# Performance work log

Measured on AMD Instinct MI355X. Metric: run time of the kernel, lower is better.

Reference implementation:

```python
import jax, jax.numpy as jnp
import numpy as np

N_PROD, N_CUST = 100000, 50000
HID, OUT = 128, 64
E_PP, E_PC, E_LB = 800000, 800000, 400000


def sage(x_src, x_dst, src, dst, Wl, bl, Wr, n_dst):
    # PyG SAGEConv (mean aggr): lin_l(mean_{j->i} x_j) + lin_r(x_i); bias on lin_l only
    msg = x_src[src]                                             # [E, d] gather
    s = jax.ops.segment_sum(msg, dst, num_segments=n_dst)        # [n_dst, d]
    cnt = jax.ops.segment_sum(jnp.ones((src.shape[0],), x_src.dtype), dst, num_segments=n_dst)
    mean = s / jnp.maximum(cnt, 1.0)[:, None]
    return mean @ Wl.T + bl + x_dst @ Wr.T


def setup_inputs() -> dict:
    key = jax.random.key(0)
    ks = iter(jax.random.split(key, 40))

    def lin_w(i, o):
        return (jax.random.normal(next(ks), (o, i), jnp.float32) / np.sqrt(i))

    inp = {}
    inp['x_product'] = jax.random.normal(next(ks), (N_PROD, HID), jnp.float32)
    inp['x_customer'] = jax.random.normal(next(ks), (N_CUST, HID), jnp.float32)
    inp['ei_pp'] = jax.random.randint(next(ks), (2, E_PP), 0, N_PROD)
    src_pc = jax.random.randint(next(ks), (1, E_PC), 0, N_PROD)
    dst_pc = jax.random.randint(next(ks), (1, E_PC), 0, N_CUST)
    inp['ei_pc'] = jnp.concatenate([src_pc, dst_pc], axis=0)
    row = jax.random.randint(next(ks), (1, E_LB), 0, N_CUST)
    col = jax.random.randint(next(ks), (1, E_LB), 0, N_PROD)
    inp['edge_label_index'] = jnp.concatenate([row, col], axis=0)

    # ItemGNNEncoder params
    inp['it_W1l'], inp['it_W1r'] = lin_w(HID, HID), lin_w(HID, HID)
    inp['it_b1'] = jnp.zeros((HID,), jnp.float32)
    inp['it_W2l'], inp['it_W2r'] = lin_w(HID, HID), lin_w(HID, HID)
    inp['it_b2'] = jnp.zeros((HID,), jnp.float32)
    inp['it_Wlin'] = lin_w(HID, OUT)
    inp['it_blin'] = jnp.zeros((OUT,), jnp.float32)
    # UserGNNEncoder params
    inp['us_W1l'], inp['us_W1r'] = lin_w(HID, HID), lin_w(HID, HID)
    inp['us_b1'] = jnp.zeros((HID,), jnp.float32)
    inp['us_W2l'], inp['us_W2r'] = lin_w(HID, HID), lin_w(HID, HID)
    inp['us_b2'] = jnp.zeros((HID,), jnp.float32)
    inp['us_W3l'], inp['us_W3r'] = lin_w(HID, HID), lin_w(HID, HID)
    inp['us_b3'] = jnp.zeros((HID,), jnp.float32)
    inp['us_Wlin'] = lin_w(HID, OUT)
    inp['us_blin'] = jnp.zeros((OUT,), jnp.float32)
    # EdgeDecoder params
    inp['de_W1'] = lin_w(2 * OUT, OUT)
    inp['de_b1'] = jnp.zeros((OUT,), jnp.float32)
    inp['de_W2'] = lin_w(OUT, 1)
    inp['de_b2'] = jnp.zeros((1,), jnp.float32)
    return inp


def reference(x_product, x_customer, ei_pp, ei_pc, edge_label_index,
              it_W1l, it_b1, it_W1r, it_W2l, it_b2, it_W2r, it_Wlin, it_blin,
              us_W1l, us_b1, us_W1r, us_W2l, us_b2, us_W2r, us_W3l, us_b3, us_W3r,
              us_Wlin, us_blin, de_W1, de_b1, de_W2, de_b2):
    pp_s, pp_d = ei_pp[0], ei_pp[1]
    pc_s, pc_d = ei_pc[0], ei_pc[1]

    # ItemGNNEncoder on product-product metapath
    p = jax.nn.relu(sage(x_product, x_product, pp_s, pp_d, it_W1l, it_b1, it_W1r, N_PROD))
    p = jax.nn.relu(sage(p, p, pp_s, pp_d, it_W2l, it_b2, it_W2r, N_PROD))
    z_prod = p @ it_Wlin.T + it_blin                              # [N_PROD, OUT]

    # UserGNNEncoder
    px = jax.nn.relu(sage(x_product, x_product, pp_s, pp_d, us_W1l, us_b1, us_W1r, N_PROD))
    cx = jax.nn.relu(sage(x_product, x_customer, pc_s, pc_d, us_W2l, us_b2, us_W2r, N_CUST))
    cx = jax.nn.relu(sage(px, cx, pc_s, pc_d, us_W3l, us_b3, us_W3r, N_CUST))
    z_cust = cx @ us_Wlin.T + us_blin                             # [N_CUST, OUT]

    # EdgeDecoder: gather-concat-MLP
    row, col = edge_label_index[0], edge_label_index[1]
    z = jnp.concatenate([z_cust[row], z_prod[col]], axis=-1)      # [E_LB, 2*OUT]
    z = jax.nn.relu(z @ de_W1.T + de_b1)
    return z @ de_W2.T + de_b2                                    # [E_LB, 1]
```

## Files before the change

kernel.cpp:

```cpp
#include <hip/hip_runtime.h>
#include <hip/hip_bf16.h>

#define HID   128
#define OUTD  64
#define NPROD 100000
#define NCUST 50000
#define EPP   800000
#define EPC   800000
#define ELB   400000
#define NBK   391
#define EBLK  4096
#define RCAP3 512
#define BCAP3 2560
#define CPADN 400
#define NB3   392
#define NCAST 6250

typedef __bf16 bf16x8 __attribute__((ext_vector_type(8)));
typedef float  f32x4  __attribute__((ext_vector_type(4)));
typedef unsigned short u16;
typedef unsigned int u32;

__device__ __forceinline__ float b2f(u16 u) {
  unsigned int v = ((unsigned int)u) << 16;
  float f; __builtin_memcpy(&f, &v, 4); return f;
}
__device__ __forceinline__ u16 f2b(float f) {
  __hip_bfloat16 h = __float2bfloat16(f);
  u16 u; __builtin_memcpy(&u, &h, 2); return u;
}

union Pack8 { u16 u[8]; int4 v; };

__device__ __forceinline__ int sidx(int row, int chunk) {
  return row * HID + ((chunk ^ (row & 15)) << 3);
}
__device__ __forceinline__ int sidx64(int row, int chunk) {
  return row * 64 + ((chunk ^ (row & 7)) << 3);
}

#define NJOBS 13
struct CastJobs { const float* src[NJOBS]; int n8[NJOBS]; };

__global__ __launch_bounds__(256) void k_prep(const int* __restrict__ ei_pp,
                                              const int* __restrict__ ei_pc,
                                              int* __restrict__ bfill_pp,
                                              int* __restrict__ bfill_pc,
                                              u32* __restrict__ bss_pp,
                                              u32* __restrict__ bss_pc,
                                              const float* __restrict__ x_prod,
                                              u16* __restrict__ XPB,
                                              CastJobs jobs,
                                              u16* __restrict__ wbuf) {
  __shared__ int lcnt[NBK], lstart[NBK], lfill[NBK], gbase[NBK];
  __shared__ u32 spay[EBLK];
  __shared__ u16 sbk[EBLK];
  __shared__ int wtot[4];
  const int t = threadIdx.x;
  int bid = blockIdx.x;

  if (bid >= NB3) {
    bid -= NB3;
    if (bid < NCAST) {
      int i = bid * 256 + t;
      float4 a = ((const float4*)x_prod)[2 * i];
      float4 b = ((const float4*)x_prod)[2 * i + 1];
      Pack8 p;
      p.u[0] = f2b(a.x); p.u[1] = f2b(a.y); p.u[2] = f2b(a.z); p.u[3] = f2b(a.w);
      p.u[4] = f2b(b.x); p.u[5] = f2b(b.y); p.u[6] = f2b(b.z); p.u[7] = f2b(b.w);
      ((int4*)XPB)[i] = p.v;
      return;
    }
    bid -= NCAST;
    int job = bid >> 3;
    int idx = (bid & 7) * 256 + t;
    int off8 = (job < 10) ? job * 2048 : 10 * 2048 + (job - 10) * 1024;
    if (idx >= jobs.n8[job]) return;
    const float* s = jobs.src[job];
    float4 a = ((const float4*)s)[2 * idx];
    float4 b = ((const float4*)s)[2 * idx + 1];
    Pack8 p;
    p.u[0] = f2b(a.x); p.u[1] = f2b(a.y); p.u[2] = f2b(a.z); p.u[3] = f2b(a.w);
    p.u[4] = f2b(b.x); p.u[5] = f2b(b.y); p.u[6] = f2b(b.z); p.u[7] = f2b(b.w);
    ((int4*)wbuf)[off8 + idx] = p.v;
    return;
  }

  const int lane = t & 63, wv = t >> 6;
  int xcc; asm("s_getreg_b32 %0, hwreg(HW_REG_XCC_ID)" : "=s"(xcc));
  const int rep = xcc & 7;
  const int NBLK_PP = (EPP + EBLK - 1) / EBLK;
  const bool isPP = bid < NBLK_PP;
  const int* ei = isPP ? ei_pp : ei_pc;
  const int E  = isPP ? EPP : EPC;
  const int SH = isPP ? 8 : 7;
  int* bfill = isPP ? bfill_pp : bfill_pc;
  u32* bss   = isPP ? bss_pp : bss_pc;
  const int base = (isPP ? bid : bid - NBLK_PP) * EBLK;
  const int n = min(EBLK, E - base);

  for (int j = t; j < NBK; j += 256) { lcnt[j] = 0; lfill[j] = 0; }
  __syncthreads();

  u32 pay[16]; int bk[16];
  #pragma unroll
  for (int i = 0; i < 16; ++i) {
    int idx = i * 256 + t;
    bk[i] = -1;
    if (idx < n) {
      int e = base + idx;
      int s = ei[e];
      int d = ei[E + e];
      int b = d >> SH;
      bk[i] = b;
      pay[i] = ((u32)s << SH) | (u32)(d & ((1 << SH) - 1));
      atomicAdd(&lcnt[b], 1);
    }
  }
  __syncthreads();
  {
    int a0 = (2 * t < NBK) ? lcnt[2 * t] : 0;
    int a1 = (2 * t + 1 < NBK) ? lcnt[2 * t + 1] : 0;
    int s = a0 + a1;
    #pragma unroll
    for (int d = 1; d < 64; d <<= 1) {
      int u = __shfl_up(s, d, 64);
      if (lane >= d) s += u;
    }
    if (lane == 63) wtot[wv] = s;
    __syncthreads();
    int wpre = 0;
    for (int w = 0; w < wv; ++w) wpre += wtot[w];
    int excl = s + wpre - (a0 + a1);
    if (2 * t < NBK) lstart[2 * t] = excl;
    if (2 * t + 1 < NBK) lstart[2 * t + 1] = excl + a0;
  }
  __syncthreads();
  for (int b = t; b < NBK; b += 256) {
    int c = lcnt[b];
    gbase[b] = c ? atomicAdd(&bfill[(rep * CPADN + b) << 4], c) : 0;
  }
  #pragma unroll
  for (int i = 0; i < 16; ++i) {
    if (bk[i] >= 0) {
      int pos = lstart[bk[i]] + atomicAdd(&lfill[bk[i]], 1);
      spay[pos] = pay[i];
      sbk[pos] = (u16)bk[i];
    }
  }
  __syncthreads();
  for (int i = t; i < n; i += 256) {
    int b = sbk[i];
    int slot = gbase[b] + (i - lstart[b]);
    if (slot < RCAP3)
      bss[(b * 8 + rep) * RCAP3 + slot] = spay[i];
  }
}

__global__ __launch_bounds__(256) void k_bsort2(const u32* __restrict__ bss_pp,
                                                const int* __restrict__ bfill_pp,
                                                const u32* __restrict__ bss_pc,
                                                const int* __restrict__ bfill_pc,
                                                int* __restrict__ gctr,
                                                int* __restrict__ esrc_pp,
                                                int* __restrict__ start_pp,
                                                int* __restrict__ cnt_pp,
                                                int* __restrict__ esrc_pc,
                                                int* __restrict__ start_pc,
                                                int* __restrict__ cnt_pc) {
  __shared__ u32 pairs[BCAP3];
  __shared__ int outsrc[BCAP3];
  __shared__ int lcnt[256], lstart[256], lfill[256];
  __shared__ int sh_n, sh_base, rn[8], roff[8], wtot[4];
  const int tid = threadIdx.x;
  const int lane = tid & 63, wv = tid >> 6;
  const bool isPP = (int)blockIdx.x < NBK;
  const int b = isPP ? (int)blockIdx.x : (int)blockIdx.x - NBK;
  const int K   = isPP ? 256 : 128;
  const int SHL = isPP ? 8 : 7;
  const u32* bss   = isPP ? bss_pp : bss_pc;
  const int* bfill = isPP ? bfill_pp : bfill_pc;
  int* gc    = isPP ? gctr : gctr + 1;
  int* esrc  = isPP ? esrc_pp : esrc_pc;
  int* start = isPP ? start_pp : start_pc;
  int* cnt   = isPP ? cnt_pp : cnt_pc;
  const int n_nodes = isPP ? NPROD : NCUST;

  if (tid < 8) rn[tid] = min(bfill[(tid * CPADN + b) << 4], RCAP3);
  for (int j = tid; j < K; j += 256) { lcnt[j] = 0; lfill[j] = 0; }
  __syncthreads();
  if (tid == 0) {
    int run = 0;
    for (int r = 0; r < 8; ++r) {
      roff[r] = run;
      int m = min(rn[r], BCAP3 - run);
      rn[r] = m;
      run += m;
    }
    sh_n = run;
    sh_base = atomicAdd(gc, run);
  }
  __syncthreads();
  const int n = sh_n, base = sh_base;
  const int Km1 = K - 1;
  #pragma unroll
  for (int r = 0; r < 8; ++r) {
    int m = rn[r], o = roff[r];
    for (int i = tid; i < m; i += 256) {
      u32 p = bss[(b * 8 + r) * RCAP3 + i];
      pairs[o + i] = p;
      atomicAdd(&lcnt[p & Km1], 1);
    }
  }
  __syncthreads();
  {
    int a0 = (2 * tid < K) ? lcnt[2 * tid] : 0;
    int a1 = (2 * tid + 1 < K) ? lcnt[2 * tid + 1] : 0;
    int s = a0 + a1;
    #pragma unroll
    for (int d = 1; d < 64; d <<= 1) {
      int u = __shfl_up(s, d, 64);
      if (lane >= d) s += u;
    }
    if (lane == 63) wtot[wv] = s;
    __syncthreads();
    int wpre = 0;
    for (int w = 0; w < wv; ++w) wpre += wtot[w];
    int excl = s + wpre - (a0 + a1);
    if (2 * tid < K) lstart[2 * tid] = excl;
    if (2 * tid + 1 < K) lstart[2 * tid + 1] = excl + a0;
  }
  __syncthreads();
  for (int i = tid; i < n; i += 256) {
    u32 p = pairs[i];
    int ln = p & Km1;
    int pos = lstart[ln] + atomicAdd(&lfill[ln], 1);
    outsrc[pos] = (int)(p >> SHL);
  }
  __syncthreads();
  for (int i = tid; i < n; i += 256) esrc[base + i] = outsrc[i];
  const int nb0 = b * K;
  for (int j = tid; j < K; j += 256) {
    int g = nb0 + j;
    if (g < n_nodes) { start[g] = base + lstart[j]; cnt[g] = lcnt[j]; }
  }
}

__global__ __launch_bounds__(256) void k_agg2(const int* __restrict__ es_a,
                                              const int* __restrict__ st_a,
                                              const int* __restrict__ cn_a,
                                              const u16* __restrict__ xa,
                                              u16* __restrict__ oa, int na,
                                              const int* __restrict__ es_b,
                                              const int* __restrict__ st_b,
                                              const int* __restrict__ cn_b,
                                              const u16* __restrict__ xb,
                                              u16* __restrict__ ob, int nb, int blkA) {
  const int t = threadIdx.x;
  const bool A = (int)blockIdx.x < blkA;
  const int node = (A ? (int)blockIdx.x : (int)blockIdx.x - blkA) * 16 + (t >> 4);
  const int l16 = t & 15;
  const int q4  = t & 48;
  if (node >= (A ? na : nb)) return;
  const int* esrc  = A ? es_a : es_b;
  const u16* x     = A ? xa : xb;
  u16* outm        = A ? oa : ob;
  int s0 = (A ? st_a : st_b)[node];
  int c  = (A ? cn_a : cn_b)[node];
  float acc[8] = {0.f, 0.f, 0.f, 0.f, 0.f, 0.f, 0.f, 0.f};
  for (int j0 = 0; j0 < c; j0 += 16) {
    int nch = min(16, c - j0);
    int eid = (l16 < nch) ? esrc[s0 + j0 + l16] : 0;
    int k = 0;
    for (; k + 4 <= nch; k += 4) {
      int s0i = __shfl(eid, q4 + k, 64);
      int s1i = __shfl(eid, q4 + k + 1, 64);
      int s2i = __shfl(eid, q4 + k + 2, 64);
      int s3i = __shfl(eid, q4 + k + 3, 64);
      Pack8 p0, p1, p2, p3;
      p0.v = *(const int4*)(x + (size_t)s0i * HID + l16 * 8);
      p1.v = *(const int4*)(x + (size_t)s1i * HID + l16 * 8);
      p2.v = *(const int4*)(x + (size_t)s2i * HID + l16 * 8);
      p3.v = *(const int4*)(x + (size_t)s3i * HID + l16 * 8);
      #pragma unroll
      for (int u = 0; u < 8; ++u)
        acc[u] += (b2f(p0.u[u]) + b2f(p1.u[u])) + (b2f(p2.u[u]) + b2f(p3.u[u]));
    }
    for (; k < nch; ++k) {
      int s = __shfl(eid, q4 + k, 64);
      Pack8 p;
      p.v = *(const int4*)(x + (size_t)s * HID + l16 * 8);
      #pragma unroll
      for (int u = 0; u < 8; ++u) acc[u] += b2f(p.u[u]);
    }
  }
  float inv = 1.0f / (float)max(c, 1);
  Pack8 o;
  #pragma unroll
  for (int u = 0; u < 8; ++u) o.u[u] = f2b(acc[u] * inv);
  *(int4*)(outm + (size_t)node * HID + l16 * 8) = o.v;
}

__global__ __launch_bounds__(256) void k_lay1(
    const u16* __restrict__ cxA1, const u16* __restrict__ cxW1,
    const float* __restrict__ cxA2f, const u16* __restrict__ cxW2,
    const float* __restrict__ cxBias, u16* __restrict__ cxOut, int Mcx,
    const u16* __restrict__ A1, const u16* __restrict__ A2,
    const u16* __restrict__ Wa, const u16* __restrict__ Wb,
    const u16* __restrict__ Wc, const u16* __restrict__ Wd,
    const float* __restrict__ bias1, const float* __restrict__ bias2,
    u16* __restrict__ out1, u16* __restrict__ out2, int M2o,
    int blkCx) {
  __shared__ __align__(16) u16 sA1[64 * HID];
  __shared__ __align__(16) u16 sA2[64 * HID];
  __shared__ __align__(16) u16 sW[128 * HID];
  const int tid  = threadIdx.x;
  const int lane = tid & 63;
  const int wave = tid >> 6;
  const int q    = lane >> 4;
  const int r16  = lane & 15;
  const bool isCx = (int)blockIdx.x < blkCx;

  if (isCx) {
    const int m0 = blockIdx.x * 64;
    f32x4 acc[4][2];
    #pragma unroll
    for (int i = 0; i < 4; ++i)
      #pragma unroll
      for (int j = 0; j < 2; ++j) {
        acc[i][j][0] = 0.f; acc[i][j][1] = 0.f; acc[i][j][2] = 0.f; acc[i][j][3] = 0.f;
      }
    #pragma unroll
    for (int phase = 0; phase < 2; ++phase) {
      const u16* W = phase ? cxW2 : cxW1;
      if (phase) __syncthreads();
      #pragma unroll
      for (int i = 0; i < 4; ++i) {
        int idx = i * 256 + tid;
        int rr = idx >> 4, c8 = idx & 15;
        int gr = m0 + rr;
        Pack8 p; p.v = make_int4(0, 0, 0, 0);
        if (gr < Mcx) {
          if (phase == 0) {
            p.v = *(const int4*)(cxA1 + (size_t)gr * HID + c8 * 8);
          } else {
            const float* s = cxA2f + (size_t)gr * HID + c8 * 8;
            float4 f0 = ((const float4*)s)[0], f1 = ((const float4*)s)[1];
            p.u[0] = f2b(f0.x); p.u[1] = f2b(f0.y); p.u[2] = f2b(f0.z); p.u[3] = f2b(f0.w);
            p.u[4] = f2b(f1.x); p.u[5] = f2b(f1.y); p.u[6] = f2b(f1.z); p.u[7] = f2b(f1.w);
          }
        }
        *(int4*)(sA1 + sidx(rr, c8)) = p.v;
      }
      #pragma unroll
      for (int i = 0; i < 8; ++i) {
        int idx = i * 256 + tid;
        int rr = idx >> 4, c8 = idx & 15;
        *(int4*)(sW + sidx(rr, c8)) = *(const int4*)(W + (size_t)rr * HID + c8 * 8);
      }
      __syncthreads();
      #pragma unroll
      for (int ks = 0; ks < 4; ++ks) {
        int chunk = ks * 4 + q;
        bf16x8 a[4], b[2];
        #pragma unroll
        for (int mi = 0; mi < 4; ++mi)
          a[mi] = *(const bf16x8*)(sA1 + sidx(mi * 16 + r16, chunk));
        #pragma unroll
        for (int ni = 0; ni < 2; ++ni)
          b[ni] = *(const bf16x8*)(sW + sidx(wave * 32 + ni * 16 + r16, chunk));
        #pragma unroll
        for (int mi = 0; mi < 4; ++mi)
          #pragma unroll
          for (int ni = 0; ni < 2; ++ni)
            acc[mi][ni] = __builtin_amdgcn_mfma_f32_16x16x32_bf16(a[mi], b[ni], acc[mi][ni], 0, 0, 0);
      }
    }
    #pragma unroll
    for (int ni = 0; ni < 2; ++ni) {
      int col = wave * 32 + ni * 16 + r16;
      float bv = cxBias[col];
      #pragma unroll
      for (int mi = 0; mi < 4; ++mi)
        #pragma unroll
        for (int r = 0; r < 4; ++r) {
          int gr = m0 + mi * 16 + q * 4 + r;
          if (gr < Mcx)
            cxOut[(size_t)gr * HID + col] = f2b(fmaxf(acc[mi][ni][r] + bv, 0.f));
        }
    }
    return;
  }

  const int m0 = ((int)blockIdx.x - blkCx) * 64;
  f32x4 acc1[4][2], acc2[4][2];
  #pragma unroll
  for (int i = 0; i < 4; ++i)
    #pragma unroll
    for (int j = 0; j < 2; ++j) {
      acc1[i][j][0] = 0.f; acc1[i][j][1] = 0.f; acc1[i][j][2] = 0.f; acc1[i][j][3] = 0.f;
      acc2[i][j][0] = 0.f; acc2[i][j][1] = 0.f; acc2[i][j][2] = 0.f; acc2[i][j][3] = 0.f;
    }

  #pragma unroll
  for (int i = 0; i < 4; ++i) {
    int idx = i * 256 + tid;
    int rr = idx >> 4, c8 = idx & 15;
    int gr = m0 + rr;
    Pack8 p1, p2;
    p1.v = make_int4(0, 0, 0, 0);
    p2.v = make_int4(0, 0, 0, 0);
    if (gr < M2o) {
      p1.v = *(const int4*)(A1 + (size_t)gr * HID + c8 * 8);
      p2.v = *(const int4*)(A2 + (size_t)gr * HID + c8 * 8);
    }
    *(int4*)(sA1 + sidx(rr, c8)) = p1.v;
    *(int4*)(sA2 + sidx(rr, c8)) = p2.v;
  }

  bf16x8 af[4][4];

  auto stageW = [&](const u16* W) {
    #pragma unroll
    for (int i = 0; i < 8; ++i) {
      int idx = i * 256 + tid;
      int rr = idx >> 4, c8 = idx & 15;
      *(int4*)(sW + sidx(rr, c8)) = *(const int4*)(W + (size_t)rr * HID + c8 * 8);
    }
  };
  auto loadA = [&](const u16* sA) {
    #pragma unroll
    for (int ks = 0; ks < 4; ++ks)
      #pragma unroll
      for (int mi = 0; mi < 4; ++mi)
        af[ks][mi] = *(const bf16x8*)(sA + sidx(mi * 16 + r16, ks * 4 + q));
  };
  auto mf = [&](f32x4 (&acc)[4][2]) {
    #pragma unroll
    for (int ks = 0; ks < 4; ++ks) {
      int chunk = ks * 4 + q;
      bf16x8 b[2];
      #pragma unroll
      for (int ni = 0; ni < 2; ++ni)
        b[ni] = *(const bf16x8*)(sW + sidx(wave * 32 + ni * 16 + r16, chunk));
      #pragma unroll
      for (int mi = 0; mi < 4; ++mi)
        #pragma unroll
        for (int ni = 0; ni < 2; ++ni)
          acc[mi][ni] = __builtin_amdgcn_mfma_f32_16x16x32_bf16(af[ks][mi], b[ni], acc[mi][ni], 0, 0, 0);
    }
  };

  stageW(Wa);
  __syncthreads();
  loadA(sA1);
  mf(acc1);
  __syncthreads();
  stageW(Wc);
  __syncthreads();
  mf(acc2);
  __syncthreads();
  stageW(Wb);
  __syncthreads();
  loadA(sA2);
  mf(acc1);
  __syncthreads();
  stageW(Wd);
  __syncthreads();
  mf(acc2);

  #pragma unroll
  for (int ni = 0; ni < 2; ++ni) {
    int col = wave * 32 + ni * 16 + r16;
    float bv1 = bias1[col];
    float bv2 = bias2[col];
    #pragma unroll
    for (int mi = 0; mi < 4; ++mi)
      #pragma unroll
      for (int r = 0; r < 4; ++r) {
        int gr = m0 + mi * 16 + q * 4 + r;
        if (gr < M2o) {
          out1[(size_t)gr * HID + col] = f2b(fmaxf(acc1[mi][ni][r] + bv1, 0.f));
          out2[(size_t)gr * HID + col] = f2b(fmaxf(acc2[mi][ni][r] + bv2, 0.f));
        }
      }
  }
}

__global__ __launch_bounds__(256) void k_chain2(
    const u16* __restrict__ A1a, const u16* __restrict__ W1a,
    const u16* __restrict__ A2a, const u16* __restrict__ W2a,
    const float* __restrict__ biasa, u16* __restrict__ outa, int Ma,
    const u16* __restrict__ Wlina, const float* __restrict__ blina,
    const u16* __restrict__ dW1a, const float* __restrict__ db1a,
    const u16* __restrict__ A1b, const u16* __restrict__ W1b,
    const u16* __restrict__ A2b, const u16* __restrict__ W2b,
    const float* __restrict__ biasb, u16* __restrict__ outb, int Mb,
    const u16* __restrict__ Wlinb, const float* __restrict__ blinb,
    const u16* __restrict__ dW1b, const float* __restrict__ db1b,
    int blkA) {
  __shared__ __align__(16) u16 sA[64 * HID];
  __shared__ __align__(16) u16 sW[128 * HID];
  const bool isA = (int)blockIdx.x < blkA;
  const u16* A1 = isA ? A1a : A1b;
  const u16* W1 = isA ? W1a : W1b;
  const u16* A2 = isA ? A2a : A2b;
  const u16* W2 = isA ? W2a : W2b;
  const float* bias = isA ? biasa : biasb;
  u16* out = isA ? outa : outb;
  const int M = isA ? Ma : Mb;
  const u16* Wlin = isA ? Wlina : Wlinb;
  const float* blin = isA ? blina : blinb;
  const u16* dW1 = isA ? dW1a : dW1b;
  const float* db1 = isA ? db1a : db1b;

  const int tid  = threadIdx.x;
  const int lane = tid & 63;
  const int wave = tid >> 6;
  const int q    = lane >> 4;
  const int r16  = lane & 15;
  const int m0   = (isA ? (int)blockIdx.x : (int)blockIdx.x - blkA) * 64;

  f32x4 acc[4][2];
  #pragma unroll
  for (int i = 0; i < 4; ++i)
    #pragma unroll
    for (int j = 0; j < 2; ++j) {
      acc[i][j][0] = 0.f; acc[i][j][1] = 0.f; acc[i][j][2] = 0.f; acc[i][j][3] = 0.f;
    }

  #pragma unroll
  for (int phase = 0; phase < 2; ++phase) {
    const u16* W = phase ? W2 : W1;
    const u16* A = phase ? A2 : A1;
    if (phase) __syncthreads();
    #pragma unroll
    for (int i = 0; i < 4; ++i) {
      int idx = i * 256 + tid;
      int rr = idx >> 4, c8 = idx & 15;
      int gr = m0 + rr;
      Pack8 p; p.v = make_int4(0, 0, 0, 0);
      if (gr < M) p.v = *(const int4*)(A + (size_t)gr * HID + c8 * 8);
      *(int4*)(sA + sidx(rr, c8)) = p.v;
    }
    #pragma unroll
    for (int i = 0; i < 8; ++i) {
      int idx = i * 256 + tid;
      int rr = idx >> 4, c8 = idx & 15;
      *(int4*)(sW + sidx(rr, c8)) = *(const int4*)(W + (size_t)rr * HID + c8 * 8);
    }
    __syncthreads();
    #pragma unroll
    for (int ks = 0; ks < 4; ++ks) {
      int chunk = ks * 4 + q;
      bf16x8 a[4], b[2];
      #pragma unroll
      for (int mi = 0; mi < 4; ++mi)
        a[mi] = *(const bf16x8*)(sA + sidx(mi * 16 + r16, chunk));
      #pragma unroll
      for (int ni = 0; ni < 2; ++ni)
        b[ni] = *(const bf16x8*)(sW + sidx(wave * 32 + ni * 16 + r16, chunk));
      #pragma unroll
      for (int mi = 0; mi < 4; ++mi)
        #pragma unroll
        for (int ni = 0; ni < 2; ++ni)
          acc[mi][ni] = __builtin_amdgcn_mfma_f32_16x16x32_bf16(a[mi], b[ni], acc[mi][ni], 0, 0, 0);
    }
  }

  __syncthreads();
  #pragma unroll
  for (int ni = 0; ni < 2; ++ni) {
    int col = wave * 32 + ni * 16 + r16;
    float bv = bias[col];
    #pragma unroll
    for (int mi = 0; mi < 4; ++mi)
      #pragma unroll
      for (int r = 0; r < 4; ++r) {
        int rl = mi * 16 + q * 4 + r;
        float v = fmaxf(acc[mi][ni][r] + bv, 0.f);
        sA[rl * HID + (((col >> 3) ^ (rl & 15)) << 3) + (col & 7)] = f2b(v);
      }
  }
  #pragma unroll
  for (int i = 0; i < 4; ++i) {
    int idx = i * 256 + tid;
    int rr = idx >> 4, c8 = idx & 15;
    *(int4*)(sW + sidx(rr, c8)) = *(const int4*)(Wlin + (size_t)rr * HID + c8 * 8);
  }
  #pragma unroll
  for (int i = 0; i < 2; ++i) {
    int idx = i * 256 + tid;
    int rr = idx >> 3, c8 = idx & 7;
    *(int4*)(sW + 8192 + sidx64(rr, c8)) = *(const int4*)(dW1 + (size_t)rr * HID + c8 * 8);
  }
  __syncthreads();
  f32x4 az[4];
  #pragma unroll
  for (int i = 0; i < 4; ++i) { az[i][0]=0.f; az[i][1]=0.f; az[i][2]=0.f; az[i][3]=0.f; }
  #pragma unroll
  for (int ks = 0; ks < 4; ++ks) {
    int chunk = ks * 4 + q;
    bf16x8 b = *(const bf16x8*)(sW + sidx(wave * 16 + r16, chunk));
    #pragma unroll
    for (int mi = 0; mi < 4; ++mi) {
      bf16x8 a = *(const bf16x8*)(sA + sidx(mi * 16 + r16, chunk));
      az[mi] = __builtin_amdgcn_mfma_f32_16x16x32_bf16(a, b, az[mi], 0, 0, 0);
    }
  }
  {
    int col = wave * 16 + r16;
    float bl = blin[col];
    #pragma unroll
    for (int mi = 0; mi < 4; ++mi)
      #pragma unroll
      for (int r = 0; r < 4; ++r) {
        int rl = mi * 16 + q * 4 + r;
        sW[12288 + rl * 64 + (((col >> 3) ^ (rl & 7)) << 3) + (col & 7)] = f2b(az[mi][r] + bl);
      }
  }
  __syncthreads();
  f32x4 au[4];
  #pragma unroll
  for (int i = 0; i < 4; ++i) { au[i][0]=0.f; au[i][1]=0.f; au[i][2]=0.f; au[i][3]=0.f; }
  #pragma unroll
  for (int ks = 0; ks < 2; ++ks) {
    int chunk = ks * 4 + q;
    bf16x8 b = *(const bf16x8*)(sW + 8192 + sidx64(wave * 16 + r16, chunk));
    #pragma unroll
    for (int mi = 0; mi < 4; ++mi) {
      bf16x8 a = *(const bf16x8*)(sW + 12288 + sidx64(mi * 16 + r16, chunk));
      au[mi] = __builtin_amdgcn_mfma_f32_16x16x32_bf16(a, b, au[mi], 0, 0, 0);
    }
  }
  {
    int col = wave * 16 + r16;
    float db = db1 ? db1[col] : 0.f;
    #pragma unroll
    for (int mi = 0; mi < 4; ++mi)
      #pragma unroll
      for (int r = 0; r < 4; ++r) {
        int gr = m0 + mi * 16 + q * 4 + r;
        if (gr < M) out[(size_t)gr * 64 + col] = f2b(au[mi][r] + db);
      }
  }
}

__global__ __launch_bounds__(256) void k_edge(const u16* __restrict__ U,
                                              const u16* __restrict__ V,
                                              const int* __restrict__ eli,
                                              const float* __restrict__ w2,
                                              const float* __restrict__ b2,
                                              float* __restrict__ out) {
  const int lane = threadIdx.x & 63;
  const int wave = threadIdx.x >> 6;
  const int se   = (lane >> 3);
  const int ch   = lane & 7;
  float w2c[8];
  #pragma unroll
  for (int j = 0; j < 8; ++j) w2c[j] = w2[ch * 8 + j];
  const float b2v = b2[0];
  const int e0 = blockIdx.x * 256;
  #pragma unroll
  for (int p = 0; p < 8; ++p) {
    int e = e0 + p * 32 + wave * 8 + se;
    if (e < ELB) {
      int r = eli[e];
      int c = eli[ELB + e];
      Pack8 pu, pv;
      pu.v = *(const int4*)(U + (size_t)r * 64 + ch * 8);
      pv.v = *(const int4*)(V + (size_t)c * 64 + ch * 8);
      float s = 0.f;
      #pragma unroll
      for (int j = 0; j < 8; ++j)
        s += fmaxf(b2f(pu.u[j]) + b2f(pv.u[j]), 0.f) * w2c[j];
      s += __shfl_xor(s, 1, 64);
      s += __shfl_xor(s, 2, 64);
      s += __shfl_xor(s, 4, 64);
      if (ch == 0) out[e] = s + b2v;
    }
  }
}

extern "C" void kernel_launch(void* const* d_in, const int* in_sizes, int n_in,
                              void* d_out, int out_size, void* d_ws, size_t ws_size,
                              hipStream_t stream) {
  const float* x_prod = (const float*)d_in[0];
  const float* x_cust = (const float*)d_in[1];
  const int* ei_pp    = (const int*)d_in[2];
  const int* ei_pc    = (const int*)d_in[3];
  const int* eli      = (const int*)d_in[4];

  const float *it_W1l, *it_W1r, *it_b1, *it_W2l, *it_W2r, *it_b2, *it_Wlin, *it_blin;
  const float *us_W1l, *us_W1r, *us_b1, *us_W2l, *us_W2r, *us_b2;
  const float *us_W3l, *us_W3r, *us_b3, *us_Wlin, *us_blin;
  if (in_sizes[6] == 128) {
    it_W1l  = (const float*)d_in[5];  it_b1   = (const float*)d_in[6];  it_W1r  = (const float*)d_in[7];
    it_W2l  = (const float*)d_in[8];  it_b2   = (const float*)d_in[9];  it_W2r  = (const float*)d_in[10];
    it_Wlin = (const float*)d_in[11]; it_blin = (const float*)d_in[12];
    us_W1l  = (const float*)d_in[13]; us_b1   = (const float*)d_in[14]; us_W1r  = (const float*)d_in[15];
    us_W2l  = (const float*)d_in[16]; us_b2   = (const float*)d_in[17]; us_W2r  = (const float*)d_in[18];
    us_W3l  = (const float*)d_in[19]; us_b3   = (const float*)d_in[20]; us_W3r  = (const float*)d_in[21];
    us_Wlin = (const float*)d_in[22]; us_blin = (const float*)d_in[23];
  } else {
    it_W1l  = (const float*)d_in[5];  it_W1r  = (const float*)d_in[6];  it_b1   = (const float*)d_in[7];
    it_W2l  = (const float*)d_in[8];  it_W2r  = (const float*)d_in[9];  it_b2   = (const float*)d_in[10];
    it_Wlin = (const float*)d_in[11]; it_blin = (const float*)d_in[12];
    us_W1l  = (const float*)d_in[13]; us_W1r  = (const float*)d_in[14]; us_b1   = (const float*)d_in[15];
    us_W2l  = (const float*)d_in[16]; us_W2r  = (const float*)d_in[17]; us_b2   = (const float*)d_in[18];
    us_W3l  = (const float*)d_in[19]; us_W3r  = (const float*)d_in[20]; us_b3   = (const float*)d_in[21];
    us_Wlin = (const float*)d_in[22]; us_blin = (const float*)d_in[23];
  }
  const float* de_W1 = (const float*)d_in[24];
  const float* de_b1 = (const float*)d_in[25];
  const float* de_W2 = (const float*)d_in[26];
  const float* de_b2 = (const float*)d_in[27];

  char* ws = (char*)d_ws;
  int* bfill_pp = (int*)(ws + 0);
  int* bfill_pc = (int*)(ws + 409600);
  int* gctr     = (int*)(ws + 819200);
  int* start_pp = (int*)(ws + 819264);
  int* cnt_pp   = (int*)(ws + 1219264);
  int* start_pc = (int*)(ws + 1619264);
  int* cnt_pc   = (int*)(ws + 1819264);
  int* esrc_pp  = (int*)(ws + 2019264);
  int* esrc_pc  = (int*)(ws + 5219264);
  u16* wbuf  = (u16*)(ws + 8419264);
  u16* XPB   = (u16*)(ws + 8796096);
  u16* meanb = (u16*)(ws + 34396096);
  u16* P1    = (u16*)(ws + 59996096);
  u16* meanc = (u16*)(ws + 85596096);
  u16* CX    = (u16*)(ws + 98396096);
  u32* bss_pp = (u32*)P1;
  u32* bss_pc = (u32*)(ws + 59996096 + 6553600);
  u16* PX = XPB;
  u16* U  = (u16*)esrc_pp;
  u16* V  = CX;

  u16* w_it1l = wbuf + 0 * 16384;  u16* w_it1r = wbuf + 1 * 16384;
  u16* w_it2l = wbuf + 2 * 16384;  u16* w_it2r = wbuf + 3 * 16384;
  u16* w_us1l = wbuf + 4 * 16384;  u16* w_us1r = wbuf + 5 * 16384;
  u16* w_us2l = wbuf + 6 * 16384;  u16* w_us2r = wbuf + 7 * 16384;
  u16* w_us3l = wbuf + 8 * 16384;  u16* w_us3r = wbuf + 9 * 16384;
  u16* w_itlin = wbuf + 10 * 16384;
  u16* w_uslin = wbuf + 10 * 16384 + 8192;
  u16* w_deW1  = wbuf + 10 * 16384 + 2 * 8192;

  (void)n_in; (void)out_size; (void)ws_size;

  hipMemsetAsync(d_ws, 0, 819208, stream);

  dim3 B(256);
  CastJobs jobs;
  jobs.src[0] = it_W1l;  jobs.src[1] = it_W1r;  jobs.src[2] = it_W2l;  jobs.src[3] = it_W2r;
  jobs.src[4] = us_W1l;  jobs.src[5] = us_W1r;  jobs.src[6] = us_W2l;  jobs.src[7] = us_W2r;
  jobs.src[8] = us_W3l;  jobs.src[9] = us_W3r;
  jobs.src[10] = it_Wlin; jobs.src[11] = us_Wlin; jobs.src[12] = de_W1;
  for (int i = 0; i < 10; ++i) jobs.n8[i] = 2048;
  for (int i = 10; i < 13; ++i) jobs.n8[i] = 1024;

  k_prep<<<dim3(NB3 + NCAST + NJOBS * 8), B, 0, stream>>>(
      ei_pp, ei_pc, bfill_pp, bfill_pc, bss_pp, bss_pc, x_prod, XPB, jobs, wbuf);
  k_bsort2<<<dim3(2 * NBK), B, 0, stream>>>(bss_pp, bfill_pp, bss_pc, bfill_pc, gctr,
                                            esrc_pp, start_pp, cnt_pp,
                                            esrc_pc, start_pc, cnt_pc);

  dim3 Gp((NPROD + 63) / 64), Gc((NCUST + 63) / 64);
  const int App = (NPROD + 15) / 16, Apc = (NCUST + 15) / 16;

  k_agg2<<<dim3(App + Apc), B, 0, stream>>>(esrc_pp, start_pp, cnt_pp, XPB, meanb, NPROD,
                                            esrc_pc, start_pc, cnt_pc, XPB, meanc, NCUST, App);
  k_lay1<<<dim3(782 + 1563), B, 0, stream>>>(
      meanc, w_us2l, x_cust, w_us2r, us_b2, CX, NCUST,
      meanb, XPB, w_it1l, w_it1r, w_us1l, w_us1r,
      it_b1, us_b1, P1, PX, NPROD, 782);
  k_agg2<<<dim3(App + Apc), B, 0, stream>>>(esrc_pp, start_pp, cnt_pp, P1, meanb, NPROD,
                                            esrc_pc, start_pc, cnt_pc, PX, meanc, NCUST, App);
  k_chain2<<<dim3(782 + 1563), B, 0, stream>>>(
      meanc, w_us3l, CX, w_us3r, us_b3, U, NCUST, w_uslin, us_blin, w_deW1, de_b1,
      meanb, w_it2l, P1, w_it2r, it_b2, V, NPROD, w_itlin, it_blin, w_deW1 + 64, nullptr,
      782);
  k_edge<<<dim3((ELB + 255) / 256), B, 0, stream>>>(U, V, eli, de_W2, de_b2, (float*)d_out);
}
```

Measured before the change: 478.2 us.

## Vectorize edge-index loads in prep and split aggregation into three launches

The bucketing prep kernel now has each thread load 16 consecutive edges with int4 vector reads instead of strided scalar loads. Each fused two-graph aggregation launch is replaced by three separate launches: two halves of the product-product graph and one for the product-customer graph. The split is meant to improve cache locality or load balance per launch, at the cost of extra launch overhead and lost overlap between the two graphs. The change also alters which edges each thread handles, and the int4 reads assume 16-byte alignment of the per-block base offsets.

```diff
diff --git a/kernel.cpp b/kernel.cpp
--- a/kernel.cpp
+++ b/kernel.cpp
@@ -103,18 +103,25 @@
   __syncthreads();
 
   u32 pay[16]; int bk[16];
-  #pragma unroll
-  for (int i = 0; i < 16; ++i) {
-    int idx = i * 256 + t;
-    bk[i] = -1;
-    if (idx < n) {
-      int e = base + idx;
-      int s = ei[e];
-      int d = ei[E + e];
-      int b = d >> SH;
-      bk[i] = b;
-      pay[i] = ((u32)s << SH) | (u32)(d & ((1 << SH) - 1));
-      atomicAdd(&lcnt[b], 1);
+  const int e0 = t * 16;
+  const int* srcp = ei + base;
+  const int* dstp = ei + E + base;
+  #pragma unroll
+  for (int i = 0; i < 16; ++i) bk[i] = -1;
+  if (e0 < n) {
+    #pragma unroll
+    for (int i = 0; i < 4; ++i) {
+      int4 s4 = *(const int4*)(srcp + e0 + i * 4);
+      int4 d4 = *(const int4*)(dstp + e0 + i * 4);
+      int ss[4] = {s4.x, s4.y, s4.z, s4.w};
+      int dd[4] = {d4.x, d4.y, d4.z, d4.w};
+      #pragma unroll
+      for (int j = 0; j < 4; ++j) {
+        int b = dd[j] >> SH;
+        bk[i * 4 + j] = b;
+        pay[i * 4 + j] = ((u32)ss[j] << SH) | (u32)(dd[j] & ((1 << SH) - 1));
+        atomicAdd(&lcnt[b], 1);
+      }
     }
   }
   __syncthreads();
@@ -766,17 +773,28 @@
                                             esrc_pp, start_pp, cnt_pp,
                                             esrc_pc, start_pc, cnt_pc);
 
-  dim3 Gp((NPROD + 63) / 64), Gc((NCUST + 63) / 64);
-  const int App = (NPROD + 15) / 16, Apc = (NCUST + 15) / 16;
-
-  k_agg2<<<dim3(App + Apc), B, 0, stream>>>(esrc_pp, start_pp, cnt_pp, XPB, meanb, NPROD,
-                                            esrc_pc, start_pc, cnt_pc, XPB, meanc, NCUST, App);
+  const int HALF = 50000;
+  const int GH = HALF / 16;
+  dim3 Gc((NCUST + 63) / 64);
+
+  k_agg2<<<dim3(GH), B, 0, stream>>>(esrc_pp, start_pp, cnt_pp, XPB, meanb, HALF,
+                                     esrc_pp, start_pp, cnt_pp, XPB, meanb, 0, GH);
+  k_agg2<<<dim3(GH), B, 0, stream>>>(esrc_pp, start_pp + HALF, cnt_pp + HALF, XPB,
+                                     meanb + (size_t)HALF * HID, HALF,
+                                     esrc_pp, start_pp, cnt_pp, XPB, meanb, 0, GH);
+  k_agg2<<<dim3(GH), B, 0, stream>>>(esrc_pc, start_pc, cnt_pc, XPB, meanc, NCUST,
+                                     esrc_pc, start_pc, cnt_pc, XPB, meanc, 0, GH);
   k_lay1<<<dim3(782 + 1563), B, 0, stream>>>(
       meanc, w_us2l, x_cust, w_us2r, us_b2, CX, NCUST,
       meanb, XPB, w_it1l, w_it1r, w_us1l, w_us1r,
       it_b1, us_b1, P1, PX, NPROD, 782);
-  k_agg2<<<dim3(App + Apc), B, 0, stream>>>(esrc_pp, start_pp, cnt_pp, P1, meanb, NPROD,
-                                            esrc_pc, start_pc, cnt_pc, PX, meanc, NCUST, App);
+  k_agg2<<<dim3(GH), B, 0, stream>>>(esrc_pp, start_pp, cnt_pp, P1, meanb, HALF,
+                                     esrc_pp, start_pp, cnt_pp, P1, meanb, 0, GH);
+  k_agg2<<<dim3(GH), B, 0, stream>>>(esrc_pp, start_pp + HALF, cnt_pp + HALF, P1,
+                                     meanb + (size_t)HALF * HID, HALF,
+                                     esrc_pp, start_pp, cnt_pp, P1, meanb, 0, GH);
+  k_agg2<<<dim3(GH), B, 0, stream>>>(esrc_pc, start_pc, cnt_pc, PX, meanc, NCUST,
+                                     esrc_pc, start_pc, cnt_pc, PX, meanc, 0, GH);
   k_chain2<<<dim3(782 + 1563), B, 0, stream>>>(
       meanc, w_us3l, CX, w_us3r, us_b3, U, NCUST, w_uslin, us_blin, w_deW1, de_b1,
       meanb, w_it2l, P1, w_it2r, it_b2, V, NPROD, w_itlin, it_blin, w_deW1 + 64, nullptr,
```

Result: no change. 485.9 us (+1.6%).

## Read GEMM weight fragments directly from global memory instead of LDS staging

Applied to the files above, without the earlier changes.

The dense layer kernels stop copying each 128x128 weight matrix into shared memory and instead load the B-operand MFMA fragments straight from global (L2-resident) memory. This removes the LDS staging traffic and several block-wide barriers, and it shrinks shared memory per block, which can raise occupancy. In exchange each wave issues its own global loads for the weights, with more latency exposure and redundant L2 reads. The edge bucketing prep also switches to per-thread contiguous int4 loads of the source and destination indices.

```diff
diff --git a/kernel.cpp b/kernel.cpp
--- a/kernel.cpp
+++ b/kernel.cpp
@@ -37,6 +37,10 @@
 }
 __device__ __forceinline__ int sidx64(int row, int chunk) {
   return row * 64 + ((chunk ^ (row & 7)) << 3);
+}
+
+__device__ __forceinline__ bf16x8 wfrag(const u16* __restrict__ W, int row, int chunk) {
+  return *(const bf16x8*)(W + (size_t)row * HID + chunk * 8);
 }
 
 #define NJOBS 13
@@ -103,18 +107,25 @@
   __syncthreads();
 
   u32 pay[16]; int bk[16];
-  #pragma unroll
-  for (int i = 0; i < 16; ++i) {
-    int idx = i * 256 + t;
-    bk[i] = -1;
-    if (idx < n) {
-      int e = base + idx;
-      int s = ei[e];
-      int d = ei[E + e];
-      int b = d >> SH;
-      bk[i] = b;
-      pay[i] = ((u32)s << SH) | (u32)(d & ((1 << SH) - 1));
-      atomicAdd(&lcnt[b], 1);
+  const int e0 = t * 16;
+  const int* srcp = ei + base;
+  const int* dstp = ei + E + base;
+  #pragma unroll
+  for (int i = 0; i < 16; ++i) bk[i] = -1;
+  if (e0 < n) {
+    #pragma unroll
+    for (int i = 0; i < 4; ++i) {
+      int4 s4 = *(const int4*)(srcp + e0 + i * 4);
+      int4 d4 = *(const int4*)(dstp + e0 + i * 4);
+      int ss[4] = {s4.x, s4.y, s4.z, s4.w};
+      int dd[4] = {d4.x, d4.y, d4.z, d4.w};
+      #pragma unroll
+      for (int j = 0; j < 4; ++j) {
+        int b = dd[j] >> SH;
+        bk[i * 4 + j] = b;
+        pay[i * 4 + j] = ((u32)ss[j] << SH) | (u32)(dd[j] & ((1 << SH) - 1));
+        atomicAdd(&lcnt[b], 1);
+      }
     }
   }
   __syncthreads();
@@ -313,7 +324,6 @@
     int blkCx) {
   __shared__ __align__(16) u16 sA1[64 * HID];
   __shared__ __align__(16) u16 sA2[64 * HID];
-  __shared__ __align__(16) u16 sW[128 * HID];
   const int tid  = threadIdx.x;
   const int lane = tid & 63;
   const int wave = tid >> 6;
@@ -352,12 +362,6 @@
         }
         *(int4*)(sA1 + sidx(rr, c8)) = p.v;
       }
-      #pragma unroll
-      for (int i = 0; i < 8; ++i) {
-        int idx = i * 256 + tid;
-        int rr = idx >> 4, c8 = idx & 15;
-        *(int4*)(sW + sidx(rr, c8)) = *(const int4*)(W + (size_t)rr * HID + c8 * 8);
-      }
       __syncthreads();
       #pragma unroll
       for (int ks = 0; ks < 4; ++ks) {
@@ -368,7 +372,7 @@
           a[mi] = *(const bf16x8*)(sA1 + sidx(mi * 16 + r16, chunk));
         #pragma unroll
         for (int ni = 0; ni < 2; ++ni)
-          b[ni] = *(const bf16x8*)(sW + sidx(wave * 32 + ni * 16 + r16, chunk));
+          b[ni] = wfrag(W, wave * 32 + ni * 16 + r16, chunk);
         #pragma unroll
         for (int mi = 0; mi < 4; ++mi)
           #pragma unroll
@@ -417,17 +421,10 @@
     *(int4*)(sA1 + sidx(rr, c8)) = p1.v;
     *(int4*)(sA2 + sidx(rr, c8)) = p2.v;
   }
+  __syncthreads();
 
   bf16x8 af[4][4];
 
-  auto stageW = [&](const u16* W) {
-    #pragma unroll
-    for (int i = 0; i < 8; ++i) {
-      int idx = i * 256 + tid;
-      int rr = idx >> 4, c8 = idx & 15;
-      *(int4*)(sW + sidx(rr, c8)) = *(const int4*)(W + (size_t)rr * HID + c8 * 8);
-    }
-  };
   auto loadA = [&](const u16* sA) {
     #pragma unroll
     for (int ks = 0; ks < 4; ++ks)
@@ -435,14 +432,14 @@
       for (int mi = 0; mi < 4; ++mi)
         af[ks][mi] = *(const bf16x8*)(sA + sidx(mi * 16 + r16, ks * 4 + q));
   };
-  auto mf = [&](f32x4 (&acc)[4][2]) {
+  auto mfW = [&](f32x4 (&acc)[4][2], const u16* W) {
     #pragma unroll
     for (int ks = 0; ks < 4; ++ks) {
       int chunk = ks * 4 + q;
       bf16x8 b[2];
       #pragma unroll
       for (int ni = 0; ni < 2; ++ni)
-        b[ni] = *(const bf16x8*)(sW + sidx(wave * 32 + ni * 16 + r16, chunk));
+        b[ni] = wfrag(W, wave * 32 + ni * 16 + r16, chunk);
       #pragma unroll
       for (int mi = 0; mi < 4; ++mi)
         #pragma unroll
@@ -451,23 +448,12 @@
     }
   };
 
-  stageW(Wa);
-  __syncthreads();
   loadA(sA1);
-  mf(acc1);
-  __syncthreads();
-  stageW(Wc);
-  __syncthreads();
-  mf(acc2);
-  __syncthreads();
-  stageW(Wb);
-  __syncthreads();
+  mfW(acc1, Wa);
+  mfW(acc2, Wc);
   loadA(sA2);
-  mf(acc1);
-  __syncthreads();
-  stageW(Wd);
-  __syncthreads();
-  mf(acc2);
+  mfW(acc1, Wb);
+  mfW(acc2, Wd);
 
   #pragma unroll
   for (int ni = 0; ni < 2; ++ni) {
@@ -500,7 +486,7 @@
     const u16* __restrict__ dW1b, const float* __restrict__ db1b,
     int blkA) {
   __shared__ __align__(16) u16 sA[64 * HID];
-  __shared__ __align__(16) u16 sW[128 * HID];
+  __shared__ __align__(16) u16 sZ[64 * 64];
   const bool isA = (int)blockIdx.x < blkA;
   const u16* A1 = isA ? A1a : A1b;
   const u16* W1 = isA ? W1a : W1b;
@@ -543,12 +529,6 @@
       if (gr < M) p.v = *(const int4*)(A + (size_t)gr * HID + c8 * 8);
       *(int4*)(sA + sidx(rr, c8)) = p.v;
     }
-    #pragma unroll
-    for (int i = 0; i < 8; ++i) {
-      int idx = i * 256 + tid;
-      int rr = idx >> 4, c8 = idx & 15;
-      *(int4*)(sW + sidx(rr, c8)) = *(const int4*)(W + (size_t)rr * HID + c8 * 8);
-    }
     __syncthreads();
     #pragma unroll
     for (int ks = 0; ks < 4; ++ks) {
@@ -559,7 +539,7 @@
         a[mi] = *(const bf16x8*)(sA + sidx(mi * 16 + r16, chunk));
       #pragma unroll
       for (int ni = 0; ni < 2; ++ni)
-        b[ni] = *(const bf16x8*)(sW + sidx(wave * 32 + ni * 16 + r16, chunk));
+        b[ni] = wfrag(W, wave * 32 + ni * 16 + r16, chunk);
       #pragma unroll
       for (int mi = 0; mi < 4; ++mi)
         #pragma unroll
@@ -582,18 +562,6 @@
         sA[rl * HID + (((col >> 3) ^ (rl & 15)) << 3) + (col & 7)] = f2b(v);
       }
   }
-  #pragma unroll
-  for (int i = 0; i < 4; ++i) {
-    int idx = i * 256 + tid;
-    int rr = idx >> 4, c8 = idx & 15;
-    *(int4*)(sW + sidx(rr, c8)) = *(const int4*)(Wlin + (size_t)rr * HID + c8 * 8);
-  }
-  #pragma unroll
-  for (int i = 0; i < 2; ++i) {
-    int idx = i * 256 + tid;
-    int rr = idx >> 3, c8 = idx & 7;
-    *(int4*)(sW + 8192 + sidx64(rr, c8)) = *(const int4*)(dW1 + (size_t)rr * HID + c8 * 8);
-  }
   __syncthreads();
   f32x4 az[4];
   #pragma unroll
@@ -601,7 +569,7 @@
   #pragma unroll
   for (int ks = 0; ks < 4; ++ks) {
     int chunk = ks * 4 + q;
-    bf16x8 b = *(const bf16x8*)(sW + sidx(wave * 16 + r16, chunk));
+    bf16x8 b = wfrag(Wlin, wave * 16 + r16, chunk);
     #pragma unroll
     for (int mi = 0; mi < 4; ++mi) {
       bf16x8 a = *(const bf16x8*)(sA + sidx(mi * 16 + r16, chunk));
@@ -616,7 +584,7 @@
       #pragma unroll
       for (int r = 0; r < 4; ++r) {
         int rl = mi * 16 + q * 4 + r;
-        sW[12288 + rl * 64 + (((col >> 3) ^ (rl & 7)) << 3) + (col & 7)] = f2b(az[mi][r] + bl);
+        sZ[rl * 64 + (((col >> 3) ^ (rl & 7)) << 3) + (col & 7)] = f2b(az[mi][r] + bl);
       }
   }
   __syncthreads();
@@ -626,10 +594,10 @@
   #pragma unroll
   for (int ks = 0; ks < 2; ++ks) {
     int chunk = ks * 4 + q;
-    bf16x8 b = *(const bf16x8*)(sW + 8192 + sidx64(wave * 16 + r16, chunk));
+    bf16x8 b = wfrag(dW1, wave * 16 + r16, chunk);
     #pragma unroll
     for (int mi = 0; mi < 4; ++mi) {
-      bf16x8 a = *(const bf16x8*)(sW + 12288 + sidx64(mi * 16 + r16, chunk));
+      bf16x8 a = *(const bf16x8*)(sZ + sidx64(mi * 16 + r16, chunk));
       au[mi] = __builtin_amdgcn_mfma_f32_16x16x32_bf16(a, b, au[mi], 0, 0, 0);
     }
   }
```

Measured after the change: 486.6 us. Within noise of the previous version (+1.8%).
